# Optimization experiments

Measured on AMD Instinct MI355X. Metric: run time of the kernel, lower is better.

## Reference

```python
import jax, jax.numpy as jnp
import numpy as np

B, DH, P, V, NP, K = 8, 1024, 64, 50257, 256, 8
SKEW = P * (P - 1) // 2


def setup_inputs() -> dict:
    key = jax.random.key(0)
    ks = jax.random.split(key, 24)
    f = jax.random.normal
    h_t = f(ks[0], (B, DH), jnp.float32)
    R = f(ks[1], (B, P, P), jnp.float32)
    A_t = 0.05 * (R - jnp.swapaxes(R, -1, -2))  # skew-symmetric
    B_t = f(ks[2], (B, NP, P), jnp.float32)
    E = f(ks[3], (V, P), jnp.float32)
    e_mask = f(ks[4], (B, P), jnp.float32)
    M = f(ks[5], (B, P, P), jnp.float32)
    G_tilde = jnp.eye(P) + 0.01 * jnp.einsum('bij,bkj->bik', M, M)  # SPD metric
    z0 = f(ks[6], (B, P), jnp.float32)
    s = lambda k_, sh: f(k_, sh, jnp.float32) * 0.02
    params = dict(
        WQ_w=s(ks[7], (DH, P)), WQ_b=jnp.zeros((P,)),
        WK_w=s(ks[8], (P, P)), WK_b=jnp.zeros((P,)),
        WV_w=s(ks[9], (P, P)), WV_b=jnp.zeros((P,)),
        WC_w=s(ks[10], (P, P)), WC_b=jnp.zeros((P,)),
        WO_w=s(ks[11], (DH, V)),
        WG_w=s(ks[12], (P, P)), WG_b=jnp.zeros((P,)),
        wgamma_w=s(ks[13], (DH + P + SKEW, 1)), wgamma_b=jnp.zeros((1,)),
        wmu_w=s(ks[14], (DH + P + 2, 1)), wmu_b=jnp.zeros((1,)),
        gdown_w=s(ks[15], (SKEW, P)),
        Sigma_inv=jnp.ones((P,)) * 0.1,
        hlie_w=s(ks[16], (DH, P)), hlie_b=jnp.zeros((P,)),
    )
    return dict(h_t=h_t, A_t=A_t, B_t=B_t, E=E, e_mask=e_mask,
                G_tilde=G_tilde, z0=z0, **params)


def _sq_riem(x, Y, G):
    # x: (B,p), Y: (B,n,p), G: (B,p,p) -> (B,n)
    d = Y - x[:, None, :]
    return jnp.einsum('bnp,bpq,bnq->bn', d, G, d)


def reference(h_t, A_t, B_t, E, e_mask, G_tilde, z0,
              WQ_w, WQ_b, WK_w, WK_b, WV_w, WV_b, WC_w, WC_b, WO_w,
              WG_w, WG_b, wgamma_w, wgamma_b, wmu_w, wmu_b,
              gdown_w, Sigma_inv, hlie_w, hlie_b):
    p = A_t.shape[-1]
    scale = 1.0 / jnp.sqrt(jnp.asarray(p, h_t.dtype))
    I = jnp.eye(p, dtype=A_t.dtype)
    Q_t = jnp.linalg.solve(I - A_t, jnp.broadcast_to(I + A_t, A_t.shape))  # Cayley map (B,p,p)
    q_t = h_t @ WQ_w + WQ_b                      # (B,p)
    B_rot = jnp.einsum('bnp,bpq->bnq', B_t, Q_t)  # (B,n,p)
    K_t = B_rot @ WK_w + WK_b
    V_t = B_rot @ WV_w + WV_b
    h_lie = h_t @ hlie_w + hlie_b                 # (B,p)
    omega = -0.5 * _sq_riem(h_lie, B_rot, G_tilde)  # (B,n)
    scores = jnp.einsum('bp,bnp->bn', q_t, K_t) * scale + omega
    alpha = jax.nn.softmax(scores, axis=-1)
    c_t = jnp.einsum('bn,bnp->bp', alpha, V_t)
    iu0, iu1 = jnp.triu_indices(p, k=1)
    g_t = A_t[:, iu0, iu1]                        # (B, skew_dim)
    E_gen = E @ WG_w + WG_b                       # (V,p)
    g_proj = g_t @ gdown_w                        # (B,p)
    diff = E_gen[None, :, :] - g_proj[:, None, :]  # (B,V,p)
    kappa = -jnp.sum(diff * diff * Sigma_inv, axis=-1)  # (B,V)
    base_logits = h_t @ WO_w                      # (B,V)
    c_rot = jnp.einsum('bp,bpq->bq', c_t @ WC_w + WC_b, Q_t)
    group_logits = c_rot @ E.T * scale + kappa
    gamma = jax.nn.sigmoid(jnp.concatenate([h_t, c_t, g_t], -1) @ wgamma_w + wgamma_b)
    logits = base_logits + gamma * group_logits
    pi = jax.nn.softmax(logits, axis=-1)
    topv, topi = jax.lax.top_k(pi, K)
    topp = topv / jnp.sum(topv, -1, keepdims=True)
    E_g = E[topi]                                 # (B,k,p) gather
    E_G = jnp.einsum('bkp,bpq->bkq', E_g, Q_t)
    E_exp = jnp.einsum('bk,bkp->bp', topp, E_G)
    H = -jnp.sum(pi * jnp.log(pi + 1e-12), -1, keepdims=True)
    rho = _sq_riem(h_lie, E_exp[:, None, :], G_tilde)  # (B,1)
    mu = jax.nn.sigmoid(jnp.concatenate([h_t, c_t, H, rho], -1) @ wmu_w + wmu_b)
    m_next = mu * e_mask + (1.0 - mu) * E_exp
    outer = m_next[:, :, None] * e_mask[:, None, :]
    A_next = A_t + 0.1 * (outer - jnp.swapaxes(outer, 1, 2))
    return logits, m_next, A_next
```

## Files before the change

kernel.cpp:

```cpp
#include <hip/hip_runtime.h>
#include <math.h>

#define NV    50257
#define OUT_M 402056
#define OUT_A 402568
#define SCALE 0.125f

#define WS_Q      0
#define WS_HTR    32768
#define WS_S      40960
#define WS_TV     45056
#define WS_C0     45120
#define WS_IU     45128
#define WS_HLIE   47144
#define WS_W1     47656
#define WS_S0     48168
#define WS_GH     48176
#define WS_WMAT   48192
#define WS_SC     80960
#define WS_WB     83008
#define WS_CONSTB 83520
#define WS_GAMMA  83528
#define WS_CT     83536
#define WS_P6     84048

__global__ __launch_bounds__(256) void k12_prep(
    const float* __restrict__ h_t, const float* __restrict__ A_t,
    const float* __restrict__ G_t,
    const float* __restrict__ WG_w, const float* __restrict__ WG_b,
    const float* __restrict__ Sigma_inv,
    const float* __restrict__ WQ_w, const float* __restrict__ WQ_b,
    const float* __restrict__ WK_w, const float* __restrict__ WK_b,
    const float* __restrict__ wgamma_w,
    const float* __restrict__ hlie_w, const float* __restrict__ hlie_b,
    float* __restrict__ ws)
{
    __shared__ float Ash[64][65];
    __shared__ float Gsh[64][65];
    __shared__ float hsh[1024];
    __shared__ float piv[2][132];
    __shared__ float fr[2][64];
    __shared__ float dsh[64];
    __shared__ float part[4][64], partb[4][64];
    __shared__ float qt[64], hl[64], qkv[64], ghl[64], v0[64];
    __shared__ float red64[4];
    __shared__ float scal[1];

    const int tid = threadIdx.x;
    const int blk = blockIdx.x;

    if (blk == 8) {
        const int a   = tid & 63;
        const int cb8 = __builtin_amdgcn_readfirstlane(tid >> 6);
        float* sig = hsh;
        float* bg  = hsh + 64;
        if (tid < 64) { sig[tid] = Sigma_inv[tid]; bg[tid] = WG_b[tid]; }
        __syncthreads();
        for (int idx = tid; idx < 4096; idx += 256) {
            int r = idx >> 6, c = idx & 63;
            float wv = WG_w[idx];
            Gsh[r][c] = wv;
            Ash[r][c] = wv * sig[c];
        }
        __syncthreads();
        float t8[16];
        #pragma unroll
        for (int j = 0; j < 16; ++j) t8[j] = 0.0f;
        for (int p = 0; p < 64; ++p) {
            float wv = Ash[a][p];
            #pragma unroll
            for (int jj = 0; jj < 16; ++jj) t8[jj] = fmaf(wv, Gsh[cb8*16 + jj][p], t8[jj]);
        }
        #pragma unroll
        for (int jj = 0; jj < 16; ++jj)
            ws[WS_S + a*64 + cb8*16 + jj] = t8[jj];
        if (cb8 == 0) {
            float s = 0.0f;
            for (int p = 0; p < 64; ++p) s += Ash[a][p] * bg[p];
            ws[WS_TV + a] = 2.0f * s;
        }
        if (tid == 0) {
            float c0 = 0.0f;
            for (int p = 0; p < 64; ++p) c0 += sig[p] * bg[p] * bg[p];
            ws[WS_C0] = c0;
        }
        return;
    }

    const int b  = blk;
    const int i  = tid & 63;
    const int cb = __builtin_amdgcn_readfirstlane(tid >> 6);
    const int col0 = cb * 16;

    for (int idx = tid; idx < 4096; idx += 256) {
        int r = idx >> 6, c = idx & 63;
        Ash[r][c] = A_t[b*4096 + idx];
        Gsh[r][c] = G_t[b*4096 + idx];
    }
    for (int k = tid; k < 1024; k += 256) {
        float hv = h_t[b*1024 + k];
        hsh[k] = hv;
        ws[WS_HTR + k*8 + b] = hv;
    }
    __syncthreads();

    float w[32];
    if (cb < 2) {
        #pragma unroll
        for (int jj = 0; jj < 32; ++jj) {
            int j = cb*32 + jj;
            w[jj] = (i == j ? 1.0f : 0.0f) - Ash[i][j];
        }
    } else {
        #pragma unroll
        for (int jj = 0; jj < 32; ++jj) {
            int j = (cb - 2)*32 + jj;
            w[jj] = (i == j ? 1.0f : 0.0f) + Ash[i][j];
        }
    }
    __syncthreads();

    #pragma unroll
    for (int k = 0; k < 64; ++k) {
        const int kb  = k >> 5;
        const int sel = k & 1;
        if (cb == kb) fr[sel][i] = w[k & 31];
        if (i == k) {
            #pragma unroll
            for (int q4 = 0; q4 < 8; ++q4)
                *(float4*)&piv[sel][cb*32 + q4*4] =
                    make_float4(w[q4*4], w[q4*4+1], w[q4*4+2], w[q4*4+3]);
        }
        __syncthreads();
        float pk = piv[sel][k];
        float f = (i == k) ? 0.0f : (fr[sel][i] / pk);
        #pragma unroll
        for (int jj = 0; jj < 32; ++jj)
            w[jj] -= f * piv[sel][cb*32 + jj];
    }

    if (cb == (i >> 5)) dsh[i] = w[i & 31];
    __syncthreads();
    if (cb >= 2) {
        float dinv = 1.0f / dsh[i];
        #pragma unroll
        for (int jj = 0; jj < 32; ++jj)
            Ash[i][(cb - 2)*32 + jj] = w[jj] * dinv;
    }
    __syncthreads();
    for (int idx = tid; idx < 4096; idx += 256)
        ws[WS_Q + b*4096 + idx] = Ash[idx >> 6][idx & 63];

    {
        float aq0 = 0, aq1 = 0, ah0 = 0, ah1 = 0, ag0 = 0, ag1 = 0;
        #pragma unroll 8
        for (int kk = 0; kk < 256; kk += 2) {
            int k = cb*256 + kk;
            float hv0 = hsh[k], hv1 = hsh[k + 1];
            aq0 = fmaf(hv0, WQ_w[k*64 + i], aq0);
            aq1 = fmaf(hv1, WQ_w[(k+1)*64 + i], aq1);
            ah0 = fmaf(hv0, hlie_w[k*64 + i], ah0);
            ah1 = fmaf(hv1, hlie_w[(k+1)*64 + i], ah1);
            ag0 = fmaf(hv0, wgamma_w[k], ag0);
            ag1 = fmaf(hv1, wgamma_w[k+1], ag1);
        }
        part[cb][i] = aq0 + aq1;
        partb[cb][i] = ah0 + ah1;
        if (i == 0) red64[cb] = ag0 + ag1;
    }
    __syncthreads();
    if (tid < 64) {
        qt[tid] = part[0][tid]+part[1][tid]+part[2][tid]+part[3][tid] + WQ_b[tid];
        hl[tid] = partb[0][tid]+partb[1][tid]+partb[2][tid]+partb[3][tid] + hlie_b[tid];
    }
    if (tid == 0) scal[0] = red64[0]+red64[1]+red64[2]+red64[3];
    __syncthreads();
    {
        float acc = 0;
        #pragma unroll
        for (int jj = 0; jj < 16; ++jj)
            acc = fmaf(WK_w[i*64 + col0 + jj], qt[col0 + jj], acc);
        part[cb][i] = acc;
    }
    __syncthreads();
    if (tid < 64) qkv[tid] = part[0][tid]+part[1][tid]+part[2][tid]+part[3][tid];
    __syncthreads();
    {
        float acc = 0;
        #pragma unroll
        for (int jj = 0; jj < 16; ++jj)
            acc = fmaf(Gsh[i][col0 + jj], hl[col0 + jj], acc);
        part[cb][i] = acc;
    }
    __syncthreads();
    if (tid < 64) {
        ghl[tid] = part[0][tid]+part[1][tid]+part[2][tid]+part[3][tid];
        v0[tid]  = SCALE*qkv[tid] + ghl[tid];
    }
    __syncthreads();
    {
        float acc = 0;
        #pragma unroll
        for (int jj = 0; jj < 16; ++jj)
            acc = fmaf(Ash[i][col0 + jj], v0[col0 + jj], acc);
        part[cb][i] = acc;
    }
    __syncthreads();
    if (tid < 64) {
        ws[WS_W1 + b*64 + tid]   = part[0][tid]+part[1][tid]+part[2][tid]+part[3][tid];
        ws[WS_HLIE + b*64 + tid] = hl[tid];
    }
    if (tid == 0) ws[WS_GH + b] = scal[0];
    float t[16];
    #pragma unroll
    for (int j = 0; j < 16; ++j) t[j] = 0;
    for (int r = 0; r < 64; ++r) {
        float qv = Ash[i][r];
        #pragma unroll
        for (int j = 0; j < 16; ++j) t[j] = fmaf(qv, Gsh[r][col0 + j], t[j]);
    }
    __syncthreads();
    #pragma unroll
    for (int j = 0; j < 16; ++j) Gsh[i][col0 + j] = t[j];
    __syncthreads();
    float w2r[16];
    #pragma unroll
    for (int j = 0; j < 16; ++j) w2r[j] = 0;
    for (int q = 0; q < 64; ++q) {
        float tv = Gsh[i][q];
        #pragma unroll
        for (int j = 0; j < 16; ++j) w2r[j] = fmaf(tv, Ash[col0 + j][q], w2r[j]);
    }
    #pragma unroll
    for (int j = 0; j < 16; ++j)
        ws[WS_WMAT + b*4096 + (col0 + j)*64 + i] = w2r[j];
}

__global__ __launch_bounds__(256) void k3_scores(
    const float* __restrict__ B_t, float* __restrict__ ws)
{
    __shared__ float Bsh[64][65];
    __shared__ float Wsh[64][64];
    __shared__ float w1sh[64];
    __shared__ float part[4][64];
    const int b = blockIdx.x >> 2, q4 = blockIdx.x & 3;
    const int tid = threadIdx.x, lane = tid & 63;
    const int gu = __builtin_amdgcn_readfirstlane(tid >> 6);
    const int col0 = gu * 16;
    for (int idx = tid; idx < 4096; idx += 256) {
        int r = idx >> 6, c = idx & 63;
        Bsh[r][c] = B_t[b*16384 + (q4*64 + r)*64 + c];
        Wsh[r][c] = ws[WS_WMAT + b*4096 + idx];
    }
    if (tid < 64) w1sh[tid] = ws[WS_W1 + b*64 + tid];
    __syncthreads();
    float t[16];
    #pragma unroll
    for (int j = 0; j < 16; ++j) t[j] = 0;
    for (int p = 0; p < 64; ++p) {
        float bv = Bsh[lane][p];
        #pragma unroll
        for (int j = 0; j < 16; ++j) t[j] = fmaf(bv, Wsh[p][col0 + j], t[j]);
    }
    float ps = 0;
    #pragma unroll
    for (int j = 0; j < 16; ++j) ps += (w1sh[col0+j] - 0.5f*t[j]) * Bsh[lane][col0+j];
    part[gu][lane] = ps;
    __syncthreads();
    if (tid < 64)
        ws[WS_SC + b*256 + q4*64 + tid] =
            part[0][tid]+part[1][tid]+part[2][tid]+part[3][tid];
}

__global__ __launch_bounds__(256) void k4_mid(
    const float* __restrict__ A_t, const float* __restrict__ B_t,
    const float* __restrict__ WV_w, const float* __restrict__ WV_b,
    const float* __restrict__ WC_w, const float* __restrict__ WC_b,
    const float* __restrict__ WG_w, const float* __restrict__ WG_b,
    const float* __restrict__ wgamma_w, const float* __restrict__ wgamma_b,
    const float* __restrict__ gdown_w, const float* __restrict__ Sigma_inv,
    float* __restrict__ ws)
{
    __shared__ float alpha[256], rr[256];
    __shared__ float part[4][64];
    __shared__ float cBr[64], cB[64], ct[64], cw[64], crot[64], gp[64], uv[64];
    __shared__ float gsh[2016];
    const int b = blockIdx.x, tid = threadIdx.x, lane = tid & 63;
    const int gu = __builtin_amdgcn_readfirstlane(tid >> 6);
    const int col0 = gu * 16;
    const float* Qb = ws + WS_Q + b*4096;

    for (int idx = tid; idx < 4096; idx += 256) {
        int i2 = idx >> 6, j2 = idx & 63;
        if (j2 > i2) {
            int s = i2*63 - ((i2*(i2-1)) >> 1) + (j2 - i2 - 1);
            gsh[s] = A_t[b*4096 + idx];
        }
    }
    float sv = ws[WS_SC + b*256 + tid];
    rr[tid] = sv; __syncthreads();
    for (int off = 128; off > 0; off >>= 1) { if (tid < off) rr[tid] = fmaxf(rr[tid], rr[tid+off]); __syncthreads(); }
    float smax = rr[0]; __syncthreads();
    float e = expf(sv - smax);
    rr[tid] = e; __syncthreads();
    for (int off = 128; off > 0; off >>= 1) { if (tid < off) rr[tid] += rr[tid+off]; __syncthreads(); }
    float den = rr[0]; __syncthreads();
    alpha[tid] = e / den;
    __syncthreads();
    {
        float acc = 0;
        for (int nn = 0; nn < 64; ++nn) {
            int n = gu*64 + nn;
            acc = fmaf(alpha[n], B_t[b*16384 + n*64 + lane], acc);
        }
        part[gu][lane] = acc;
    }
    __syncthreads();
    if (tid < 64) cBr[tid] = part[0][tid]+part[1][tid]+part[2][tid]+part[3][tid];
    __syncthreads();
    {
        float acc = 0;
        #pragma unroll
        for (int pp = 0; pp < 16; ++pp) { int p = col0+pp; acc = fmaf(cBr[p], Qb[p*64+lane], acc); }
        part[gu][lane] = acc;
    }
    __syncthreads();
    if (tid < 64) cB[tid] = part[0][tid]+part[1][tid]+part[2][tid]+part[3][tid];
    __syncthreads();
    {
        float acc = 0;
        #pragma unroll
        for (int pp = 0; pp < 16; ++pp) { int p = col0+pp; acc = fmaf(cB[p], WV_w[p*64+lane], acc); }
        part[gu][lane] = acc;
    }
    __syncthreads();
    if (tid < 64) {
        float v = part[0][tid]+part[1][tid]+part[2][tid]+part[3][tid] + WV_b[tid];
        ct[tid] = v; ws[WS_CT + b*64 + tid] = v;
    }
    __syncthreads();
    {
        float acc = 0;
        #pragma unroll
        for (int pp = 0; pp < 16; ++pp) { int p = col0+pp; acc = fmaf(ct[p], WC_w[p*64+lane], acc); }
        part[gu][lane] = acc;
    }
    __syncthreads();
    if (tid < 64) cw[tid] = part[0][tid]+part[1][tid]+part[2][tid]+part[3][tid] + WC_b[tid];
    __syncthreads();
    {
        float acc = 0;
        #pragma unroll
        for (int pp = 0; pp < 16; ++pp) { int p = col0+pp; acc = fmaf(cw[p], Qb[p*64+lane], acc); }
        part[gu][lane] = acc;
    }
    __syncthreads();
    if (tid < 64) crot[tid] = part[0][tid]+part[1][tid]+part[2][tid]+part[3][tid];
    __syncthreads();
    {
        float accp0 = 0, accp1 = 0, accg0 = 0, accg1 = 0;
        #pragma unroll 4
        for (int ss = 0; ss < 504; ss += 2) {
            int s = gu*504 + ss;
            float av0 = gsh[s], av1 = gsh[s + 1];
            accp0 = fmaf(av0, gdown_w[s*64 + lane], accp0);
            accp1 = fmaf(av1, gdown_w[(s+1)*64 + lane], accp1);
            accg0 = fmaf(av0, wgamma_w[1088 + s], accg0);
            accg1 = fmaf(av1, wgamma_w[1089 + s], accg1);
        }
        part[gu][lane] = accp0 + accp1;
        if (lane == 0) rr[gu] = accg0 + accg1;
    }
    if (tid < 64) rr[64 + tid] = ct[tid] * wgamma_w[1024 + tid];
    __syncthreads();
    if (tid < 64) {
        float g = part[0][tid]+part[1][tid]+part[2][tid]+part[3][tid];
        gp[tid] = g; uv[tid] = 2.0f * Sigma_inv[tid] * g;
    }
    if (tid == 0) {
        float gc = 0; for (int j = 0; j < 64; ++j) gc += rr[64 + j];
        float z = ws[WS_GH + b] + gc + rr[0]+rr[1]+rr[2]+rr[3] + wgamma_b[0];
        ws[WS_GAMMA + b] = 1.0f / (1.0f + expf(-z));
    }
    __syncthreads();
    {
        float acc = 0;
        #pragma unroll
        for (int pp = 0; pp < 16; ++pp) { int p = col0+pp; acc = fmaf(WG_w[lane*64+p], uv[p], acc); }
        part[gu][lane] = acc;
    }
    if (tid < 64) rr[tid] = WG_b[tid]*uv[tid] - gp[tid]*gp[tid]*Sigma_inv[tid];
    __syncthreads();
    if (tid < 64)
        ws[WS_WB + b*64 + tid] = SCALE*crot[tid]
            + part[0][tid]+part[1][tid]+part[2][tid]+part[3][tid];
    if (tid == 0) { float s = 0; for (int j = 0; j < 64; ++j) s += rr[j]; ws[WS_CONSTB + b] = s; }
}

#define KU 16
__global__ __launch_bounds__(256) void k5_logits(
    const float* __restrict__ E, const float* __restrict__ WO_w,
    const float* __restrict__ ws, float* __restrict__ out)
{
    __shared__ float smem[14544];
    const int tid  = threadIdx.x;
    const int half = tid >> 7;
    const int vt   = tid & 127;
    const int vb = blockIdx.x * 128;
    const int v = vb + vt;
    const bool vok = v < NV;
    const int vv = vok ? v : NV - 1;

    float* Esh  = smem;
    float* Ssh  = smem + 8448;
    float* tvsh = smem + 12544;
    float* wbsh = smem + 12608;
    float* gmsh = smem + 13120;
    float* cbsh = smem + 13128;
    float* svsh = smem + 13136;
    float* gdsh = smem + 13392;

    for (int idx = tid; idx < 2048; idx += 256) {
        int r = idx >> 4, c4 = (idx & 15) * 4;
        int vr = vb + r; if (vr >= NV) vr = NV - 1;
        float4 e4 = *(const float4*)(E + (size_t)vr * 64 + c4);
        float* dst = Esh + r*66 + c4;
        dst[0] = e4.x; dst[1] = e4.y; dst[2] = e4.z; dst[3] = e4.w;
    }
    for (int idx = tid; idx < 4096; idx += 256) Ssh[idx] = ws[WS_S + idx];
    for (int idx = tid; idx < 512; idx += 256) wbsh[idx] = ws[WS_WB + idx];
    if (tid < 64) tvsh[tid] = ws[WS_TV + tid];
    if (tid < 8) { gmsh[tid] = ws[WS_GAMMA + tid]; cbsh[tid] = ws[WS_CONSTB + tid]; }
    __syncthreads();
    {
        const float* er = Esh + vt*66;
        float sv = (half == 0) ? ws[WS_C0] : 0.0f;
        #pragma unroll
        for (int jj = 0; jj < 2; ++jj) {
            const int jb = half*2 + jj;
            float t[16];
            #pragma unroll
            for (int j = 0; j < 16; ++j) t[j] = 0.0f;
            for (int p = 0; p < 64; ++p) {
                float ep = er[p];
                #pragma unroll
                for (int j = 0; j < 16; ++j)
                    t[j] = fmaf(ep, Ssh[p*64 + jb*16 + j], t[j]);
            }
            #pragma unroll
            for (int j = 0; j < 16; ++j)
                sv += (t[j] + tvsh[jb*16 + j]) * er[jb*16 + j];
        }
        svsh[half*128 + vt] = sv;
        const float* w0 = wbsh + (half*4    )*64;
        const float* w1 = wbsh + (half*4 + 1)*64;
        const float* w2 = wbsh + (half*4 + 2)*64;
        const float* w3 = wbsh + (half*4 + 3)*64;
        float g0 = 0, g1 = 0, g2 = 0, g3 = 0;
        #pragma unroll 8
        for (int p = 0; p < 64; ++p) {
            float ep = er[p];
            g0 = fmaf(ep, w0[p], g0); g1 = fmaf(ep, w1[p], g1);
            g2 = fmaf(ep, w2[p], g2); g3 = fmaf(ep, w3[p], g3);
        }
        float* gr = gdsh + vt*9 + half*4;
        gr[0] = g0; gr[1] = g1; gr[2] = g2; gr[3] = g3;
    }
    __syncthreads();
    float* hsh   = smem;
    float* accsh = smem + 8192;
    for (int idx = tid; idx < 8192; idx += 256) hsh[idx] = ws[WS_HTR + idx];
    __syncthreads();
    float acc[8];
    #pragma unroll
    for (int bb = 0; bb < 8; ++bb) acc[bb] = 0.0f;
    {
        const float* wo = WO_w + (size_t)(half * 512) * NV + vv;
        const float* hb = hsh + half*512*8;
        for (int k0 = 0; k0 < 512; k0 += KU) {
            float wr[KU];
            #pragma unroll
            for (int u = 0; u < KU; ++u) wr[u] = wo[(size_t)(k0 + u) * NV];
            #pragma unroll
            for (int u = 0; u < KU; ++u) {
                const float* hp = hb + (k0 + u)*8;
                #pragma unroll
                for (int bb = 0; bb < 8; ++bb) acc[bb] = fmaf(hp[bb], wr[u], acc[bb]);
            }
        }
    }
    if (half == 1) {
        float* ar = accsh + vt*9;
        #pragma unroll
        for (int bb = 0; bb < 8; ++bb) ar[bb] = acc[bb];
    }
    __syncthreads();
    if (half == 0 && vok) {
        const float* ar = accsh + vt*9;
        const float* gr = gdsh + vt*9;
        float svt = svsh[vt] + svsh[128 + vt];
        #pragma unroll
        for (int bb = 0; bb < 8; ++bb) {
            float gl = gr[bb] + cbsh[bb] - svt;
            out[bb*NV + v] = fmaf(gmsh[bb], gl, acc[bb] + ar[bb]);
        }
    }
}

#define NQ 12565
__global__ __launch_bounds__(256) void k6a_scan(
    const float* __restrict__ outl, float* __restrict__ ws)
{
    __shared__ float candv[2048];
    __shared__ int   candi[2048];
    __shared__ float redv[256];
    __shared__ int   redi[256];
    __shared__ int   redo[256];
    __shared__ float sred[256];
    __shared__ float t8v[8];
    __shared__ int   t8i[8];
    __shared__ int   iscal[1];
    const int b = blockIdx.x >> 2, q = blockIdx.x & 3;
    const int tid = threadIdx.x;
    const int v0 = q * NQ;
    const int v1 = (v0 + NQ < NV) ? (v0 + NQ) : NV;
    const float* lg = outl + b*NV;

    float lv[8]; int li[8];
    #pragma unroll
    for (int u = 0; u < 8; ++u) { lv[u] = -INFINITY; li[u] = 0x7fffffff; }
    for (int v = v0 + tid; v < v1; v += 256) {
        float x = lg[v];
        if (x > lv[7]) {
            int p = 7;
            while (p > 0 && x > lv[p-1]) { lv[p] = lv[p-1]; li[p] = li[p-1]; --p; }
            lv[p] = x; li[p] = v;
        }
    }
    #pragma unroll
    for (int u = 0; u < 8; ++u) { candv[tid*8 + u] = lv[u]; candi[tid*8 + u] = li[u]; }
    __syncthreads();
    int ptr = 0;
    for (int it = 0; it < 8; ++it) {
        redv[tid] = (ptr < 8) ? candv[tid*8 + ptr] : -INFINITY;
        redi[tid] = (ptr < 8) ? candi[tid*8 + ptr] : 0x7fffffff;
        redo[tid] = tid;
        __syncthreads();
        for (int off = 128; off > 0; off >>= 1) {
            if (tid < off) {
                float ov = redv[tid + off]; int oi = redi[tid + off];
                if (ov > redv[tid] || (ov == redv[tid] && oi < redi[tid])) {
                    redv[tid] = ov; redi[tid] = oi; redo[tid] = redo[tid + off];
                }
            }
            __syncthreads();
        }
        if (tid == 0) { t8v[it] = redv[0]; t8i[it] = redi[0]; iscal[0] = redo[0]; }
        __syncthreads();
        if (tid == iscal[0]) ++ptr;
        __syncthreads();
    }
    float Mp = t8v[0];
    float s1 = 0, s2 = 0;
    for (int v = v0 + tid; v < v1; v += 256) {
        float x = lg[v];
        float ee = expf(x - Mp);
        s1 += ee; s2 += x * ee;
    }
    redv[tid] = s1; sred[tid] = s2;
    __syncthreads();
    for (int off = 128; off > 0; off >>= 1) {
        if (tid < off) { redv[tid] += redv[tid+off]; sred[tid] += sred[tid+off]; }
        __syncthreads();
    }
    if (tid == 0) {
        int base = WS_P6 + (b*4 + q)*20;
        #pragma unroll
        for (int u = 0; u < 8; ++u) { ws[base + u] = t8v[u]; ((int*)ws)[base + 8 + u] = t8i[u]; }
        ws[base + 16] = Mp; ws[base + 17] = redv[0]; ws[base + 18] = sred[0];
    }
}

__global__ __launch_bounds__(256) void k6b_final(
    const float* __restrict__ h_t, const float* __restrict__ A_t,
    const float* __restrict__ E, const float* __restrict__ e_mask,
    const float* __restrict__ G_t,
    const float* __restrict__ wmu_w, const float* __restrict__ wmu_b,
    const float* __restrict__ ws, float* __restrict__ out)
{
    __shared__ float mv[32];
    __shared__ int   mi[32];
    __shared__ float t8v[8];
    __shared__ int   t8i[8];
    __shared__ float toppsh[8];
    __shared__ float redv[256];
    __shared__ float uvec[64], eexp[64], msh[64], emsh[64];
    __shared__ float scal[4];
    const int b = blockIdx.x, tid = threadIdx.x;

    if (tid < 32) {
        int base = WS_P6 + (b*4 + (tid >> 3))*20;
        mv[tid] = ws[base + (tid & 7)];
        mi[tid] = ((const int*)ws)[base + 8 + (tid & 7)];
    }
    __syncthreads();
    if (tid == 0) {
        unsigned used = 0;
        for (int it = 0; it < 8; ++it) {
            float best = -INFINITY; int bi = 0x7fffffff, bs = 0;
            for (int c = 0; c < 32; ++c) {
                if (used & (1u << c)) continue;
                float x = mv[c];
                if (x > best || (x == best && mi[c] < bi)) { best = x; bi = mi[c]; bs = c; }
            }
            used |= 1u << bs; t8v[it] = best; t8i[it] = bi;
        }
        float M = t8v[0];
        float s1 = 0, s2 = 0;
        for (int q = 0; q < 4; ++q) {
            int base = WS_P6 + (b*4 + q)*20;
            float sc_ = expf(ws[base + 16] - M);
            s1 += ws[base + 17] * sc_; s2 += ws[base + 18] * sc_;
        }
        scal[0] = M + logf(s1) - s2 / s1;
        float ts = 0, tv_[8];
        #pragma unroll
        for (int u = 0; u < 8; ++u) { tv_[u] = expf(t8v[u] - M); ts += tv_[u]; }
        #pragma unroll
        for (int u = 0; u < 8; ++u) toppsh[u] = tv_[u] / ts;
    }
    __syncthreads();
    if (tid < 64) {
        float u_ = 0;
        #pragma unroll
        for (int j = 0; j < 8; ++j) u_ += toppsh[j] * E[t8i[j]*64 + tid];
        uvec[tid] = u_;
    }
    __syncthreads();
    if (tid < 64) {
        const float* Qb = ws + WS_Q + b*4096;
        float a = 0;
        for (int p = 0; p < 64; ++p) a += uvec[p] * Qb[p*64 + tid];
        eexp[tid] = a;
    }
    __syncthreads();
    {
        const float* Gb = G_t + b*4096;
        const float* HL = ws + WS_HLIE + b*64;
        float a = 0;
        #pragma unroll 4
        for (int t2 = 0; t2 < 16; ++t2) {
            int idx = tid*16 + t2;
            int p = idx >> 6, q = idx & 63;
            a += (eexp[p] - HL[p]) * Gb[idx] * (eexp[q] - HL[q]);
        }
        redv[tid] = a;
    }
    __syncthreads();
    for (int off = 128; off > 0; off >>= 1) {
        if (tid < off) redv[tid] += redv[tid + off];
        __syncthreads();
    }
    if (tid == 0) scal[1] = redv[0];
    __syncthreads();
    float pm = 0;
    for (int k = tid; k < 1024; k += 256) pm += h_t[b*1024 + k] * wmu_w[k];
    if (tid < 64) pm += ws[WS_CT + b*64 + tid] * wmu_w[1024 + tid];
    redv[tid] = pm;
    __syncthreads();
    for (int off = 128; off > 0; off >>= 1) {
        if (tid < off) redv[tid] += redv[tid + off];
        __syncthreads();
    }
    if (tid == 0) {
        float z = redv[0] + scal[0]*wmu_w[1088] + scal[1]*wmu_w[1089] + wmu_b[0];
        scal[2] = 1.0f / (1.0f + expf(-z));
    }
    __syncthreads();
    if (tid < 64) {
        float mu = scal[2];
        float em = e_mask[b*64 + tid];
        float m = mu*em + (1.0f - mu)*eexp[tid];
        out[OUT_M + b*64 + tid] = m;
        msh[tid] = m; emsh[tid] = em;
    }
    __syncthreads();
    for (int idx = tid; idx < 4096; idx += 256) {
        int i = idx >> 6, j = idx & 63;
        out[OUT_A + b*4096 + idx] = A_t[b*4096 + idx]
            + 0.1f*(msh[i]*emsh[j] - msh[j]*emsh[i]);
    }
}

extern "C" void kernel_launch(void* const* d_in, const int* in_sizes, int n_in,
                              void* d_out, int out_size, void* d_ws, size_t ws_size,
                              hipStream_t stream)
{
    const float* h_t      = (const float*)d_in[0];
    const float* A_t      = (const float*)d_in[1];
    const float* B_t      = (const float*)d_in[2];
    const float* E        = (const float*)d_in[3];
    const float* e_mask   = (const float*)d_in[4];
    const float* G_t      = (const float*)d_in[5];
    const float* WQ_w     = (const float*)d_in[7];
    const float* WQ_b     = (const float*)d_in[8];
    const float* WK_w     = (const float*)d_in[9];
    const float* WK_b     = (const float*)d_in[10];
    const float* WV_w     = (const float*)d_in[11];
    const float* WV_b     = (const float*)d_in[12];
    const float* WC_w     = (const float*)d_in[13];
    const float* WC_b     = (const float*)d_in[14];
    const float* WO_w     = (const float*)d_in[15];
    const float* WG_w     = (const float*)d_in[16];
    const float* WG_b     = (const float*)d_in[17];
    const float* wgamma_w = (const float*)d_in[18];
    const float* wgamma_b = (const float*)d_in[19];
    const float* wmu_w    = (const float*)d_in[20];
    const float* wmu_b    = (const float*)d_in[21];
    const float* gdown_w  = (const float*)d_in[22];
    const float* Sigma_inv= (const float*)d_in[23];
    const float* hlie_w   = (const float*)d_in[24];
    const float* hlie_b   = (const float*)d_in[25];
    float* out = (float*)d_out;
    float* ws  = (float*)d_ws;

    k12_prep<<<9, 256, 0, stream>>>(h_t, A_t, G_t, WG_w, WG_b, Sigma_inv,
                                    WQ_w, WQ_b, WK_w, WK_b, wgamma_w,
                                    hlie_w, hlie_b, ws);
    k3_scores<<<32, 256, 0, stream>>>(B_t, ws);
    k4_mid<<<8, 256, 0, stream>>>(A_t, B_t, WV_w, WV_b, WC_w, WC_b, WG_w, WG_b,
                                  wgamma_w, wgamma_b, gdown_w, Sigma_inv, ws);
    k5_logits<<<393, 256, 0, stream>>>(E, WO_w, ws, out);
    k6a_scan<<<32, 256, 0, stream>>>(out, ws);
    k6b_final<<<8, 256, 0, stream>>>(h_t, A_t, E, e_mask, G_t, wmu_w, wmu_b, ws, out);
}
```

Measured before the change: 551.0 us.

## Fuse prep, scores and mid kernels; widen logits grid; single-pass top-k scan

Merges the three small per-batch kernels (prep, attention scores, mid) into one kernel per batch. Intermediate matrices such as the rotation Q, W1 and the score matrix now stay in shared memory instead of round-tripping through the workspace, and two launches disappear. The logits kernel now handles 64 vocab columns per block with a 4-way split over K, doubling the grid for better occupancy, at the cost of a cross-wave reduction. The top-k/softmax scan computes max, sums and top-8 in one pass with online rescaling and wavefront shuffles instead of repeated block reductions. The fused kernel serialises the score work on only 8 blocks, which may lengthen that stage.

```diff
diff --git a/kernel.cpp b/kernel.cpp
--- a/kernel.cpp
+++ b/kernel.cpp
@@ -11,39 +11,41 @@
 #define WS_S      40960
 #define WS_TV     45056
 #define WS_C0     45120
-#define WS_IU     45128
 #define WS_HLIE   47144
-#define WS_W1     47656
-#define WS_S0     48168
 #define WS_GH     48176
-#define WS_WMAT   48192
-#define WS_SC     80960
 #define WS_WB     83008
 #define WS_CONSTB 83520
 #define WS_GAMMA  83528
 #define WS_CT     83536
 #define WS_P6     84048
 
-__global__ __launch_bounds__(256) void k12_prep(
+__global__ __launch_bounds__(256) void k_batch(
     const float* __restrict__ h_t, const float* __restrict__ A_t,
-    const float* __restrict__ G_t,
+    const float* __restrict__ G_t, const float* __restrict__ B_t,
     const float* __restrict__ WG_w, const float* __restrict__ WG_b,
     const float* __restrict__ Sigma_inv,
     const float* __restrict__ WQ_w, const float* __restrict__ WQ_b,
-    const float* __restrict__ WK_w, const float* __restrict__ WK_b,
-    const float* __restrict__ wgamma_w,
+    const float* __restrict__ WK_w,
+    const float* __restrict__ WV_w, const float* __restrict__ WV_b,
+    const float* __restrict__ WC_w, const float* __restrict__ WC_b,
+    const float* __restrict__ wgamma_w, const float* __restrict__ wgamma_b,
+    const float* __restrict__ gdown_w,
     const float* __restrict__ hlie_w, const float* __restrict__ hlie_b,
     float* __restrict__ ws)
 {
     __shared__ float Ash[64][65];
     __shared__ float Gsh[64][65];
+    __shared__ float Bq[64][65];
     __shared__ float hsh[1024];
     __shared__ float piv[2][132];
     __shared__ float fr[2][64];
     __shared__ float dsh[64];
     __shared__ float part[4][64], partb[4][64];
-    __shared__ float qt[64], hl[64], qkv[64], ghl[64], v0[64];
-    __shared__ float red64[4];
+    __shared__ float qt[64], hl[64], qkv[64], ghl[64], v0[64], w1sh[64];
+    __shared__ float sc[256], rr[256];
+    __shared__ float cBr[64], cB[64], ct[64], cw[64], crot[64], gp[64], uv[64];
+    __shared__ float gsh[2016];
+    __shared__ float red4[4];
     __shared__ float scal[1];
 
     const int tid = threadIdx.x;
@@ -104,6 +106,14 @@
     }
     __syncthreads();
 
+    for (int idx = tid; idx < 4096; idx += 256) {
+        int i2 = idx >> 6, j2 = idx & 63;
+        if (j2 > i2) {
+            int s = i2*63 - ((i2*(i2-1)) >> 1) + (j2 - i2 - 1);
+            gsh[s] = Ash[i2][j2];
+        }
+    }
+
     float w[32];
     if (cb < 2) {
         #pragma unroll
@@ -166,14 +176,14 @@
         }
         part[cb][i] = aq0 + aq1;
         partb[cb][i] = ah0 + ah1;
-        if (i == 0) red64[cb] = ag0 + ag1;
+        if (i == 0) red4[cb] = ag0 + ag1;
     }
     __syncthreads();
     if (tid < 64) {
         qt[tid] = part[0][tid]+part[1][tid]+part[2][tid]+part[3][tid] + WQ_b[tid];
         hl[tid] = partb[0][tid]+partb[1][tid]+partb[2][tid]+partb[3][tid] + hlie_b[tid];
     }
-    if (tid == 0) scal[0] = red64[0]+red64[1]+red64[2]+red64[3];
+    if (tid == 0) scal[0] = red4[0]+red4[1]+red4[2]+red4[3];
     __syncthreads();
     {
         float acc = 0;
@@ -207,21 +217,20 @@
     }
     __syncthreads();
     if (tid < 64) {
-        ws[WS_W1 + b*64 + tid]   = part[0][tid]+part[1][tid]+part[2][tid]+part[3][tid];
+        w1sh[tid] = part[0][tid]+part[1][tid]+part[2][tid]+part[3][tid];
         ws[WS_HLIE + b*64 + tid] = hl[tid];
     }
-    if (tid == 0) ws[WS_GH + b] = scal[0];
-    float t[16];
-    #pragma unroll
-    for (int j = 0; j < 16; ++j) t[j] = 0;
+    float tt[16];
+    #pragma unroll
+    for (int j = 0; j < 16; ++j) tt[j] = 0;
     for (int r = 0; r < 64; ++r) {
         float qv = Ash[i][r];
         #pragma unroll
-        for (int j = 0; j < 16; ++j) t[j] = fmaf(qv, Gsh[r][col0 + j], t[j]);
-    }
-    __syncthreads();
-    #pragma unroll
-    for (int j = 0; j < 16; ++j) Gsh[i][col0 + j] = t[j];
+        for (int j = 0; j < 16; ++j) tt[j] = fmaf(qv, Gsh[r][col0 + j], tt[j]);
+    }
+    __syncthreads();
+    #pragma unroll
+    for (int j = 0; j < 16; ++j) Gsh[i][col0 + j] = tt[j];
     __syncthreads();
     float w2r[16];
     #pragma unroll
@@ -231,89 +240,53 @@
         #pragma unroll
         for (int j = 0; j < 16; ++j) w2r[j] = fmaf(tv, Ash[col0 + j][q], w2r[j]);
     }
-    #pragma unroll
-    for (int j = 0; j < 16; ++j)
-        ws[WS_WMAT + b*4096 + (col0 + j)*64 + i] = w2r[j];
-}
-
-__global__ __launch_bounds__(256) void k3_scores(
-    const float* __restrict__ B_t, float* __restrict__ ws)
-{
-    __shared__ float Bsh[64][65];
-    __shared__ float Wsh[64][64];
-    __shared__ float w1sh[64];
-    __shared__ float part[4][64];
-    const int b = blockIdx.x >> 2, q4 = blockIdx.x & 3;
-    const int tid = threadIdx.x, lane = tid & 63;
-    const int gu = __builtin_amdgcn_readfirstlane(tid >> 6);
-    const int col0 = gu * 16;
-    for (int idx = tid; idx < 4096; idx += 256) {
-        int r = idx >> 6, c = idx & 63;
-        Bsh[r][c] = B_t[b*16384 + (q4*64 + r)*64 + c];
-        Wsh[r][c] = ws[WS_WMAT + b*4096 + idx];
-    }
-    if (tid < 64) w1sh[tid] = ws[WS_W1 + b*64 + tid];
-    __syncthreads();
-    float t[16];
-    #pragma unroll
-    for (int j = 0; j < 16; ++j) t[j] = 0;
-    for (int p = 0; p < 64; ++p) {
-        float bv = Bsh[lane][p];
-        #pragma unroll
-        for (int j = 0; j < 16; ++j) t[j] = fmaf(bv, Wsh[p][col0 + j], t[j]);
-    }
-    float ps = 0;
-    #pragma unroll
-    for (int j = 0; j < 16; ++j) ps += (w1sh[col0+j] - 0.5f*t[j]) * Bsh[lane][col0+j];
-    part[gu][lane] = ps;
-    __syncthreads();
-    if (tid < 64)
-        ws[WS_SC + b*256 + q4*64 + tid] =
-            part[0][tid]+part[1][tid]+part[2][tid]+part[3][tid];
-}
-
-__global__ __launch_bounds__(256) void k4_mid(
-    const float* __restrict__ A_t, const float* __restrict__ B_t,
-    const float* __restrict__ WV_w, const float* __restrict__ WV_b,
-    const float* __restrict__ WC_w, const float* __restrict__ WC_b,
-    const float* __restrict__ WG_w, const float* __restrict__ WG_b,
-    const float* __restrict__ wgamma_w, const float* __restrict__ wgamma_b,
-    const float* __restrict__ gdown_w, const float* __restrict__ Sigma_inv,
-    float* __restrict__ ws)
-{
-    __shared__ float alpha[256], rr[256];
-    __shared__ float part[4][64];
-    __shared__ float cBr[64], cB[64], ct[64], cw[64], crot[64], gp[64], uv[64];
-    __shared__ float gsh[2016];
-    const int b = blockIdx.x, tid = threadIdx.x, lane = tid & 63;
-    const int gu = __builtin_amdgcn_readfirstlane(tid >> 6);
-    const int col0 = gu * 16;
-    const float* Qb = ws + WS_Q + b*4096;
-
-    for (int idx = tid; idx < 4096; idx += 256) {
-        int i2 = idx >> 6, j2 = idx & 63;
-        if (j2 > i2) {
-            int s = i2*63 - ((i2*(i2-1)) >> 1) + (j2 - i2 - 1);
-            gsh[s] = A_t[b*4096 + idx];
-        }
-    }
-    float sv = ws[WS_SC + b*256 + tid];
-    rr[tid] = sv; __syncthreads();
+    __syncthreads();
+    #pragma unroll
+    for (int j = 0; j < 16; ++j) Gsh[col0 + j][i] = w2r[j];
+    __syncthreads();
+
+    for (int q4 = 0; q4 < 4; ++q4) {
+        for (int idx = tid; idx < 4096; idx += 256) {
+            int r = idx >> 6, c = idx & 63;
+            Bq[r][c] = B_t[b*16384 + (q4*64 + r)*64 + c];
+        }
+        __syncthreads();
+        float ts[16];
+        #pragma unroll
+        for (int j = 0; j < 16; ++j) ts[j] = 0;
+        for (int p = 0; p < 64; ++p) {
+            float bv = Bq[i][p];
+            #pragma unroll
+            for (int j = 0; j < 16; ++j) ts[j] = fmaf(bv, Gsh[p][col0 + j], ts[j]);
+        }
+        float ps = 0;
+        #pragma unroll
+        for (int j = 0; j < 16; ++j)
+            ps += (w1sh[col0+j] - 0.5f*ts[j]) * Bq[i][col0+j];
+        part[cb][i] = ps;
+        __syncthreads();
+        if (tid < 64)
+            sc[q4*64 + tid] = part[0][tid]+part[1][tid]+part[2][tid]+part[3][tid];
+        __syncthreads();
+    }
+
+    float svv = sc[tid];
+    rr[tid] = svv; __syncthreads();
     for (int off = 128; off > 0; off >>= 1) { if (tid < off) rr[tid] = fmaxf(rr[tid], rr[tid+off]); __syncthreads(); }
     float smax = rr[0]; __syncthreads();
-    float e = expf(sv - smax);
+    float e = expf(svv - smax);
     rr[tid] = e; __syncthreads();
     for (int off = 128; off > 0; off >>= 1) { if (tid < off) rr[tid] += rr[tid+off]; __syncthreads(); }
     float den = rr[0]; __syncthreads();
-    alpha[tid] = e / den;
+    sc[tid] = e / den;
     __syncthreads();
     {
         float acc = 0;
         for (int nn = 0; nn < 64; ++nn) {
-            int n = gu*64 + nn;
-            acc = fmaf(alpha[n], B_t[b*16384 + n*64 + lane], acc);
-        }
-        part[gu][lane] = acc;
+            int n = cb*64 + nn;
+            acc = fmaf(sc[n], B_t[b*16384 + n*64 + i], acc);
+        }
+        part[cb][i] = acc;
     }
     __syncthreads();
     if (tid < 64) cBr[tid] = part[0][tid]+part[1][tid]+part[2][tid]+part[3][tid];
@@ -321,8 +294,8 @@
     {
         float acc = 0;
         #pragma unroll
-        for (int pp = 0; pp < 16; ++pp) { int p = col0+pp; acc = fmaf(cBr[p], Qb[p*64+lane], acc); }
-        part[gu][lane] = acc;
+        for (int pp = 0; pp < 16; ++pp) { int p = col0+pp; acc = fmaf(cBr[p], Ash[p][i], acc); }
+        part[cb][i] = acc;
     }
     __syncthreads();
     if (tid < 64) cB[tid] = part[0][tid]+part[1][tid]+part[2][tid]+part[3][tid];
@@ -330,8 +303,8 @@
     {
         float acc = 0;
         #pragma unroll
-        for (int pp = 0; pp < 16; ++pp) { int p = col0+pp; acc = fmaf(cB[p], WV_w[p*64+lane], acc); }
-        part[gu][lane] = acc;
+        for (int pp = 0; pp < 16; ++pp) { int p = col0+pp; acc = fmaf(cB[p], WV_w[p*64+i], acc); }
+        part[cb][i] = acc;
     }
     __syncthreads();
     if (tid < 64) {
@@ -342,8 +315,8 @@
     {
         float acc = 0;
         #pragma unroll
-        for (int pp = 0; pp < 16; ++pp) { int p = col0+pp; acc = fmaf(ct[p], WC_w[p*64+lane], acc); }
-        part[gu][lane] = acc;
+        for (int pp = 0; pp < 16; ++pp) { int p = col0+pp; acc = fmaf(ct[p], WC_w[p*64+i], acc); }
+        part[cb][i] = acc;
     }
     __syncthreads();
     if (tid < 64) cw[tid] = part[0][tid]+part[1][tid]+part[2][tid]+part[3][tid] + WC_b[tid];
@@ -351,8 +324,8 @@
     {
         float acc = 0;
         #pragma unroll
-        for (int pp = 0; pp < 16; ++pp) { int p = col0+pp; acc = fmaf(cw[p], Qb[p*64+lane], acc); }
-        part[gu][lane] = acc;
+        for (int pp = 0; pp < 16; ++pp) { int p = col0+pp; acc = fmaf(cw[p], Ash[p][i], acc); }
+        part[cb][i] = acc;
     }
     __syncthreads();
     if (tid < 64) crot[tid] = part[0][tid]+part[1][tid]+part[2][tid]+part[3][tid];
@@ -361,15 +334,15 @@
         float accp0 = 0, accp1 = 0, accg0 = 0, accg1 = 0;
         #pragma unroll 4
         for (int ss = 0; ss < 504; ss += 2) {
-            int s = gu*504 + ss;
+            int s = cb*504 + ss;
             float av0 = gsh[s], av1 = gsh[s + 1];
-            accp0 = fmaf(av0, gdown_w[s*64 + lane], accp0);
-            accp1 = fmaf(av1, gdown_w[(s+1)*64 + lane], accp1);
+            accp0 = fmaf(av0, gdown_w[s*64 + i], accp0);
+            accp1 = fmaf(av1, gdown_w[(s+1)*64 + i], accp1);
             accg0 = fmaf(av0, wgamma_w[1088 + s], accg0);
             accg1 = fmaf(av1, wgamma_w[1089 + s], accg1);
         }
-        part[gu][lane] = accp0 + accp1;
-        if (lane == 0) rr[gu] = accg0 + accg1;
+        part[cb][i] = accp0 + accp1;
+        if (i == 0) rr[cb] = accg0 + accg1;
     }
     if (tid < 64) rr[64 + tid] = ct[tid] * wgamma_w[1024 + tid];
     __syncthreads();
@@ -379,15 +352,15 @@
     }
     if (tid == 0) {
         float gc = 0; for (int j = 0; j < 64; ++j) gc += rr[64 + j];
-        float z = ws[WS_GH + b] + gc + rr[0]+rr[1]+rr[2]+rr[3] + wgamma_b[0];
+        float z = scal[0] + gc + rr[0]+rr[1]+rr[2]+rr[3] + wgamma_b[0];
         ws[WS_GAMMA + b] = 1.0f / (1.0f + expf(-z));
     }
     __syncthreads();
     {
         float acc = 0;
         #pragma unroll
-        for (int pp = 0; pp < 16; ++pp) { int p = col0+pp; acc = fmaf(WG_w[lane*64+p], uv[p], acc); }
-        part[gu][lane] = acc;
+        for (int pp = 0; pp < 16; ++pp) { int p = col0+pp; acc = fmaf(WG_w[i*64+p], uv[p], acc); }
+        part[cb][i] = acc;
     }
     if (tid < 64) rr[tid] = WG_b[tid]*uv[tid] - gp[tid]*gp[tid]*Sigma_inv[tid];
     __syncthreads();
@@ -402,25 +375,27 @@
     const float* __restrict__ E, const float* __restrict__ WO_w,
     const float* __restrict__ ws, float* __restrict__ out)
 {
-    __shared__ float smem[14544];
-    const int tid  = threadIdx.x;
-    const int half = tid >> 7;
-    const int vt   = tid & 127;
-    const int vb = blockIdx.x * 128;
-    const int v = vb + vt;
+    __shared__ float smem[11600];
+    const int tid = threadIdx.x;
+    const int q   = tid >> 6;
+    const int vt  = tid & 63;
+    const int vb  = blockIdx.x * 64;
+    const int v   = vb + vt;
     const bool vok = v < NV;
     const int vv = vok ? v : NV - 1;
 
     float* Esh  = smem;
-    float* Ssh  = smem + 8448;
-    float* tvsh = smem + 12544;
-    float* wbsh = smem + 12608;
-    float* gmsh = smem + 13120;
-    float* cbsh = smem + 13128;
-    float* svsh = smem + 13136;
-    float* gdsh = smem + 13392;
-
-    for (int idx = tid; idx < 2048; idx += 256) {
+    float* Ssh  = smem + 4224;
+    float* tvsh = smem + 8448;
+    float* wbsh = smem + 8512;
+    float* gmsh = smem + 9024;
+    float* cbsh = smem + 9032;
+    float* svsh = smem + 9040;
+    float* gdsh = smem + 9296;
+    float* accsh= smem + 9872;
+    float* hsh  = smem;
+
+    for (int idx = tid; idx < 1024; idx += 256) {
         int r = idx >> 4, c4 = (idx & 15) * 4;
         int vr = vb + r; if (vr >= NV) vr = NV - 1;
         float4 e4 = *(const float4*)(E + (size_t)vr * 64 + c4);
@@ -434,10 +409,8 @@
     __syncthreads();
     {
         const float* er = Esh + vt*66;
-        float sv = (half == 0) ? ws[WS_C0] : 0.0f;
-        #pragma unroll
-        for (int jj = 0; jj < 2; ++jj) {
-            const int jb = half*2 + jj;
+        float sv = (q == 0) ? ws[WS_C0] : 0.0f;
+        {
             float t[16];
             #pragma unroll
             for (int j = 0; j < 16; ++j) t[j] = 0.0f;
@@ -445,39 +418,35 @@
                 float ep = er[p];
                 #pragma unroll
                 for (int j = 0; j < 16; ++j)
-                    t[j] = fmaf(ep, Ssh[p*64 + jb*16 + j], t[j]);
+                    t[j] = fmaf(ep, Ssh[p*64 + q*16 + j], t[j]);
             }
             #pragma unroll
             for (int j = 0; j < 16; ++j)
-                sv += (t[j] + tvsh[jb*16 + j]) * er[jb*16 + j];
-        }
-        svsh[half*128 + vt] = sv;
-        const float* w0 = wbsh + (half*4    )*64;
-        const float* w1 = wbsh + (half*4 + 1)*64;
-        const float* w2 = wbsh + (half*4 + 2)*64;
-        const float* w3 = wbsh + (half*4 + 3)*64;
-        float g0 = 0, g1 = 0, g2 = 0, g3 = 0;
+                sv += (t[j] + tvsh[q*16 + j]) * er[q*16 + j];
+        }
+        svsh[q*64 + vt] = sv;
+        const float* w0 = wbsh + (2*q    )*64;
+        const float* w1 = wbsh + (2*q + 1)*64;
+        float g0 = 0, g1 = 0;
         #pragma unroll 8
         for (int p = 0; p < 64; ++p) {
             float ep = er[p];
             g0 = fmaf(ep, w0[p], g0); g1 = fmaf(ep, w1[p], g1);
-            g2 = fmaf(ep, w2[p], g2); g3 = fmaf(ep, w3[p], g3);
-        }
-        float* gr = gdsh + vt*9 + half*4;
-        gr[0] = g0; gr[1] = g1; gr[2] = g2; gr[3] = g3;
-    }
-    __syncthreads();
-    float* hsh   = smem;
-    float* accsh = smem + 8192;
-    for (int idx = tid; idx < 8192; idx += 256) hsh[idx] = ws[WS_HTR + idx];
+        }
+        gdsh[vt*9 + 2*q]     = g0;
+        gdsh[vt*9 + 2*q + 1] = g1;
+    }
+    __syncthreads();
+    for (int idx = tid; idx < 2048; idx += 256)
+        *(float4*)(hsh + idx*4) = *(const float4*)(ws + WS_HTR + idx*4);
     __syncthreads();
     float acc[8];
     #pragma unroll
     for (int bb = 0; bb < 8; ++bb) acc[bb] = 0.0f;
     {
-        const float* wo = WO_w + (size_t)(half * 512) * NV + vv;
-        const float* hb = hsh + half*512*8;
-        for (int k0 = 0; k0 < 512; k0 += KU) {
+        const float* wo = WO_w + (size_t)(q * 256) * NV + vv;
+        const float* hb = hsh + q*256*8;
+        for (int k0 = 0; k0 < 256; k0 += KU) {
             float wr[KU];
             #pragma unroll
             for (int u = 0; u < KU; ++u) wr[u] = wo[(size_t)(k0 + u) * NV];
@@ -489,20 +458,20 @@
             }
         }
     }
-    if (half == 1) {
-        float* ar = accsh + vt*9;
+    if (q) {
+        float* ar = accsh + (q-1)*576 + vt*9;
         #pragma unroll
         for (int bb = 0; bb < 8; ++bb) ar[bb] = acc[bb];
     }
     __syncthreads();
-    if (half == 0 && vok) {
-        const float* ar = accsh + vt*9;
+    if (q == 0 && vok) {
+        float svt = svsh[vt] + svsh[64+vt] + svsh[128+vt] + svsh[192+vt];
         const float* gr = gdsh + vt*9;
-        float svt = svsh[vt] + svsh[128 + vt];
         #pragma unroll
         for (int bb = 0; bb < 8; ++bb) {
+            float a = acc[bb] + accsh[vt*9+bb] + accsh[576+vt*9+bb] + accsh[1152+vt*9+bb];
             float gl = gr[bb] + cbsh[bb] - svt;
-            out[bb*NV + v] = fmaf(gmsh[bb], gl, acc[bb] + ar[bb]);
+            out[bb*NV + v] = fmaf(gmsh[bb], gl, a);
         }
     }
 }
@@ -511,73 +480,96 @@
 __global__ __launch_bounds__(256) void k6a_scan(
     const float* __restrict__ outl, float* __restrict__ ws)
 {
-    __shared__ float candv[2048];
-    __shared__ int   candi[2048];
-    __shared__ float redv[256];
-    __shared__ int   redi[256];
-    __shared__ int   redo[256];
-    __shared__ float sred[256];
+    __shared__ float mvw[4][8];
+    __shared__ int   miw[4][8];
     __shared__ float t8v[8];
     __shared__ int   t8i[8];
-    __shared__ int   iscal[1];
-    const int b = blockIdx.x >> 2, q = blockIdx.x & 3;
-    const int tid = threadIdx.x;
-    const int v0 = q * NQ;
+    __shared__ float redv[4], sred[4];
+    const int b = blockIdx.x >> 2, qq = blockIdx.x & 3;
+    const int tid = threadIdx.x, lane = tid & 63, wvi = tid >> 6;
+    const int v0 = qq * NQ;
     const int v1 = (v0 + NQ < NV) ? (v0 + NQ) : NV;
     const float* lg = outl + b*NV;
 
     float lv[8]; int li[8];
     #pragma unroll
     for (int u = 0; u < 8; ++u) { lv[u] = -INFINITY; li[u] = 0x7fffffff; }
+    float mt = -INFINITY, s1 = 0.0f, s2 = 0.0f;
     for (int v = v0 + tid; v < v1; v += 256) {
         float x = lg[v];
+        if (x > mt) {
+            float r = expf(mt - x);
+            s1 *= r; s2 *= r; mt = x;
+        }
+        float ee = expf(x - mt);
+        s1 += ee; s2 += x * ee;
         if (x > lv[7]) {
-            int p = 7;
-            while (p > 0 && x > lv[p-1]) { lv[p] = lv[p-1]; li[p] = li[p-1]; --p; }
-            lv[p] = x; li[p] = v;
-        }
-    }
-    #pragma unroll
-    for (int u = 0; u < 8; ++u) { candv[tid*8 + u] = lv[u]; candi[tid*8 + u] = li[u]; }
-    __syncthreads();
-    int ptr = 0;
-    for (int it = 0; it < 8; ++it) {
-        redv[tid] = (ptr < 8) ? candv[tid*8 + ptr] : -INFINITY;
-        redi[tid] = (ptr < 8) ? candi[tid*8 + ptr] : 0x7fffffff;
-        redo[tid] = tid;
-        __syncthreads();
-        for (int off = 128; off > 0; off >>= 1) {
-            if (tid < off) {
-                float ov = redv[tid + off]; int oi = redi[tid + off];
-                if (ov > redv[tid] || (ov == redv[tid] && oi < redi[tid])) {
-                    redv[tid] = ov; redi[tid] = oi; redo[tid] = redo[tid + off];
+            float cv = x; int ci = v;
+            #pragma unroll
+            for (int u = 0; u < 8; ++u) {
+                if (cv > lv[u]) {
+                    float tv = lv[u]; lv[u] = cv; cv = tv;
+                    int   ti = li[u]; li[u] = ci; ci = ti;
                 }
             }
-            __syncthreads();
-        }
-        if (tid == 0) { t8v[it] = redv[0]; t8i[it] = redi[0]; iscal[0] = redo[0]; }
-        __syncthreads();
-        if (tid == iscal[0]) ++ptr;
-        __syncthreads();
-    }
+        }
+    }
+    float wv8[8]; int wi8[8];
+    #pragma unroll
+    for (int it = 0; it < 8; ++it) {
+        float bv = lv[0]; int bi = li[0];
+        #pragma unroll
+        for (int off = 32; off > 0; off >>= 1) {
+            float ov = __shfl_xor(bv, off);
+            int   oi = __shfl_xor(bi, off);
+            if (ov > bv || (ov == bv && oi < bi)) { bv = ov; bi = oi; }
+        }
+        wv8[it] = bv; wi8[it] = bi;
+        if (lv[0] == bv && li[0] == bi) {
+            lv[0]=lv[1]; lv[1]=lv[2]; lv[2]=lv[3]; lv[3]=lv[4];
+            lv[4]=lv[5]; lv[5]=lv[6]; lv[6]=lv[7]; lv[7]=-INFINITY;
+            li[0]=li[1]; li[1]=li[2]; li[2]=li[3]; li[3]=li[4];
+            li[4]=li[5]; li[5]=li[6]; li[6]=li[7]; li[7]=0x7fffffff;
+        }
+    }
+    if (lane == 0) {
+        #pragma unroll
+        for (int u = 0; u < 8; ++u) { mvw[wvi][u] = wv8[u]; miw[wvi][u] = wi8[u]; }
+    }
+    __syncthreads();
+    if (tid == 0) {
+        int pA = 0, pB = 0, pC = 0, pD = 0;
+        for (int it = 0; it < 8; ++it) {
+            float vA = mvw[0][pA], vB = mvw[1][pB], vC = mvw[2][pC], vD = mvw[3][pD];
+            int   iA = miw[0][pA], iB = miw[1][pB], iC = miw[2][pC], iD = miw[3][pD];
+            float best = vA; int bi = iA; int w = 0;
+            if (vB > best || (vB == best && iB < bi)) { best = vB; bi = iB; w = 1; }
+            if (vC > best || (vC == best && iC < bi)) { best = vC; bi = iC; w = 2; }
+            if (vD > best || (vD == best && iD < bi)) { best = vD; bi = iD; w = 3; }
+            t8v[it] = best; t8i[it] = bi;
+            if (w == 0) ++pA; else if (w == 1) ++pB; else if (w == 2) ++pC; else ++pD;
+        }
+    }
+    __syncthreads();
     float Mp = t8v[0];
-    float s1 = 0, s2 = 0;
-    for (int v = v0 + tid; v < v1; v += 256) {
-        float x = lg[v];
-        float ee = expf(x - Mp);
-        s1 += ee; s2 += x * ee;
-    }
-    redv[tid] = s1; sred[tid] = s2;
-    __syncthreads();
-    for (int off = 128; off > 0; off >>= 1) {
-        if (tid < off) { redv[tid] += redv[tid+off]; sred[tid] += sred[tid+off]; }
-        __syncthreads();
-    }
+    {
+        float r = expf(mt - Mp);
+        s1 *= r; s2 *= r;
+    }
+    #pragma unroll
+    for (int off = 32; off > 0; off >>= 1) {
+        s1 += __shfl_xor(s1, off);
+        s2 += __shfl_xor(s2, off);
+    }
+    if (lane == 0) { redv[wvi] = s1; sred[wvi] = s2; }
+    __syncthreads();
     if (tid == 0) {
-        int base = WS_P6 + (b*4 + q)*20;
+        int base = WS_P6 + (b*4 + qq)*20;
         #pragma unroll
         for (int u = 0; u < 8; ++u) { ws[base + u] = t8v[u]; ((int*)ws)[base + 8 + u] = t8i[u]; }
-        ws[base + 16] = Mp; ws[base + 17] = redv[0]; ws[base + 18] = sred[0];
+        ws[base + 16] = Mp;
+        ws[base + 17] = redv[0]+redv[1]+redv[2]+redv[3];
+        ws[base + 18] = sred[0]+sred[1]+sred[2]+sred[3];
     }
 }
 
@@ -705,7 +697,6 @@
     const float* WQ_w     = (const float*)d_in[7];
     const float* WQ_b     = (const float*)d_in[8];
     const float* WK_w     = (const float*)d_in[9];
-    const float* WK_b     = (const float*)d_in[10];
     const float* WV_w     = (const float*)d_in[11];
     const float* WV_b     = (const float*)d_in[12];
     const float* WC_w     = (const float*)d_in[13];
@@ -724,13 +715,11 @@
     float* out = (float*)d_out;
     float* ws  = (float*)d_ws;
 
-    k12_prep<<<9, 256, 0, stream>>>(h_t, A_t, G_t, WG_w, WG_b, Sigma_inv,
-                                    WQ_w, WQ_b, WK_w, WK_b, wgamma_w,
-                                    hlie_w, hlie_b, ws);
-    k3_scores<<<32, 256, 0, stream>>>(B_t, ws);
-    k4_mid<<<8, 256, 0, stream>>>(A_t, B_t, WV_w, WV_b, WC_w, WC_b, WG_w, WG_b,
-                                  wgamma_w, wgamma_b, gdown_w, Sigma_inv, ws);
-    k5_logits<<<393, 256, 0, stream>>>(E, WO_w, ws, out);
+    k_batch<<<9, 256, 0, stream>>>(h_t, A_t, G_t, B_t, WG_w, WG_b, Sigma_inv,
+                                   WQ_w, WQ_b, WK_w, WV_w, WV_b, WC_w, WC_b,
+                                   wgamma_w, wgamma_b, gdown_w,
+                                   hlie_w, hlie_b, ws);
+    k5_logits<<<786, 256, 0, stream>>>(E, WO_w, ws, out);
     k6a_scan<<<32, 256, 0, stream>>>(out, ws);
     k6b_final<<<8, 256, 0, stream>>>(h_t, A_t, E, e_mask, G_t, wmu_w, wmu_b, ws, out);
 }
```

Measured after the change: 582.2 us. +5.7%, slower.
